# Kernel optimization log

Hardware: AMD Instinct MI355X
Metric: run time of the kernel (lower is better)

The kernel has to match this reference:

```python
import jax, jax.numpy as jnp
import numpy as np


def setup_inputs() -> dict:
    key = jax.random.key(0)
    ks = jax.random.split(key, 7)
    B, N, D = 32, 512, 64
    H = D // 2
    return {
        "receiver": jax.random.normal(ks[0], (B, N, D), dtype=jnp.float32),
        "attendant": jax.random.normal(ks[1], (B, N, D), dtype=jnp.float32),
        "adj_mask": jax.random.uniform(ks[2], (B, N, N), dtype=jnp.float32),
        "w_q": jax.random.normal(ks[3], (D, H), dtype=jnp.float32) * (1.0 / np.sqrt(D)),
        "w_k": jax.random.normal(ks[4], (D, H), dtype=jnp.float32) * (1.0 / np.sqrt(D)),
        "bias": jax.random.normal(ks[5], (H,), dtype=jnp.float32) * 0.1,
        "a": jax.random.normal(ks[6], (H,), dtype=jnp.float32) * 0.1,
    }


def reference(receiver, attendant, adj_mask, w_q, w_k, bias, a):
    # keys: [B,N,H], queries: [B,N,H]
    keys = receiver @ w_k
    queries = attendant @ w_q
    # additive (GAT-style) scores: broadcast-add -> tanh -> dot with a
    # e_act: [B, N, M, H]  (N from keys, M from queries, matching torch unsqueeze(-3)/(-2))
    e_act = jnp.tanh(queries[:, None, :, :] + keys[:, :, None, :] + bias)
    e_scores = jnp.einsum("bnmh,h->bnm", e_act, a)
    # masked projection: adj @ scores @ adj
    att = jnp.einsum("bnk,bkm->bnm", adj_mask, e_scores)
    att = jnp.einsum("bnk,bkm->bnm", att, adj_mask)
    return att
```

## Files before the change

kernel.cpp:

```cpp
#include <hip/hip_runtime.h>

#define GN 512
#define HH 32
#define DD 64

typedef float v4f __attribute__((ext_vector_type(4)));
typedef unsigned int v4u __attribute__((ext_vector_type(4)));
typedef u_int32_t u32;
typedef u32 v2u __attribute__((ext_vector_type(2)));
typedef __bf16 v8bf __attribute__((ext_vector_type(8)));

__device__ __forceinline__ u32 f2bf(float f) {
  u32 u = __builtin_bit_cast(u32, f);
  return (u + 0x7fffu + ((u >> 16) & 1u)) >> 16;
}
__device__ __forceinline__ u32 pack2(float a, float b) {
  return f2bf(a) | (f2bf(b) << 16);
}

#define GLOAD16(g, l)                                                              \
  __builtin_amdgcn_global_load_lds((const __attribute__((address_space(1))) u32*)(g), \
                                   (__attribute__((address_space(3))) u32*)(l), 16, 0, 0)
#define VMCNT0 asm volatile("s_waitcnt vmcnt(0)" ::: "memory")

__global__ __launch_bounds__(256) void kq_kernel(const float* __restrict__ rec,
                                                 const float* __restrict__ att,
                                                 const float* __restrict__ wq,
                                                 const float* __restrict__ wk,
                                                 const float* __restrict__ bias,
                                                 float* __restrict__ ekbuf,
                                                 float* __restrict__ eqbuf) {
  __shared__ float rr[512], ra[512];
  int tid = threadIdx.x;
  size_t base = (size_t)blockIdx.x * 8;
  const float* gr = rec + base * DD;
  const float* ga = att + base * DD;
  rr[tid] = gr[tid]; rr[tid + 256] = gr[tid + 256];
  ra[tid] = ga[tid]; ra[tid + 256] = ga[tid + 256];
  __syncthreads();
  int r = tid >> 5, h = tid & 31;
  float sk = bias[h], sq = 0.f;
  const float* rrow = &rr[r * DD];
  const float* arow = &ra[r * DD];
#pragma unroll 8
  for (int d = 0; d < DD; ++d) {
    sk += rrow[d] * wk[d * HH + h];
    sq += arow[d] * wq[d * HH + h];
  }
  const float C = 2.8853900817779268f;
  ekbuf[(base + r) * HH + h] = __builtin_exp2f(C * sk);
  eqbuf[(base + r) * HH + h] = __builtin_exp2f(C * sq);
}

__global__ __launch_bounds__(256) void prep_kernel(const float* __restrict__ adj,
                                                   const float* __restrict__ ek,
                                                   const float* __restrict__ eq,
                                                   const float* __restrict__ avec,
                                                   unsigned short* __restrict__ adjT,
                                                   unsigned short* __restrict__ adjBF,
                                                   unsigned short* __restrict__ Et) {
  __shared__ __align__(16) float smem[4608];
  float (*t)[65] = (float (*)[65])smem;
  float (*kl)[36] = (float (*)[36])smem;
  float (*ql)[36] = (float (*)[36])&smem[64 * 36];

  int tid = threadIdx.x;
  int b = blockIdx.z;
  int n0 = blockIdx.x * 64, m0 = blockIdx.y * 64;
  int c0 = n0, r0 = m0;

  const float* kb = ek + ((size_t)b * GN + n0) * HH;
  const float* qb = eq + ((size_t)b * GN + m0) * HH;
  v4f rk[2], rq[2];
#pragma unroll
  for (int k = 0; k < 2; ++k) {
    int v = tid + k * 256;
    int row = v >> 3, seg = v & 7;
    rk[k] = *(const v4f*)(kb + row * HH + seg * 4);
    rq[k] = *(const v4f*)(qb + row * HH + seg * 4);
  }
  v4f a2v[8];
  float asum = 0.f;
#pragma unroll
  for (int h4 = 0; h4 < 8; ++h4) {
    v4f av = *(const v4f*)(avec + h4 * 4);
    a2v[h4] = av * 2.0f;
    asum += av[0] + av[1] + av[2] + av[3];
  }

  const float* ab = adj + (size_t)b * GN * GN;
  unsigned short* ob = adjT + (size_t)b * GN * GN;
  unsigned short* of = adjBF + (size_t)b * GN * GN;
#pragma unroll
  for (int k = 0; k < 4; ++k) {
    int v = tid + k * 256;
    int row = v >> 4, seg = v & 15;
    v4f f = *(const v4f*)(ab + (size_t)(r0 + row) * GN + c0 + seg * 4);
    t[row][seg * 4 + 0] = f[0];
    t[row][seg * 4 + 1] = f[1];
    t[row][seg * 4 + 2] = f[2];
    t[row][seg * 4 + 3] = f[3];
    v2u p = {pack2(f[0], f[1]), pack2(f[2], f[3])};
    *(v2u*)(of + (size_t)(r0 + row) * GN + c0 + seg * 4) = p;
  }
  __syncthreads();
  {
    int c = tid >> 2;
    int rs = (tid & 3) * 16;
    v4u p0, p1;
#pragma unroll
    for (int j = 0; j < 4; ++j) {
      p0[j] = pack2(t[rs + 2 * j][c], t[rs + 2 * j + 1][c]);
      p1[j] = pack2(t[rs + 8 + 2 * j][c], t[rs + 9 + 2 * j][c]);
    }
    unsigned short* dst = ob + (size_t)(c0 + c) * GN + r0 + rs;
    *(v4u*)dst = p0;
    *(v4u*)(dst + 8) = p1;
  }
  __syncthreads();

#pragma unroll
  for (int k = 0; k < 2; ++k) {
    int v = tid + k * 256;
    int row = v >> 3, seg = v & 7;
    *(v4f*)&kl[row][seg * 4] = rk[k];
    *(v4f*)&ql[row][seg * 4] = rq[k];
  }
  __syncthreads();
  int m = tid >> 2, ng = tid & 3;
  v4f qv[8];
#pragma unroll
  for (int h4 = 0; h4 < 8; ++h4) qv[h4] = *(const v4f*)&ql[m][h4 * 4];
  u32* dstw = (u32*)(Et + ((size_t)b * GN + m0 + m) * GN + n0);
#pragma unroll 4
  for (int nn = 0; nn < 8; ++nn) {
    int n = ng * 2 + nn * 8;
    v4f acc0 = (v4f){0.f, 0.f, 0.f, 0.f};
    v4f acc1 = (v4f){0.f, 0.f, 0.f, 0.f};
#pragma unroll
    for (int h4 = 0; h4 < 8; ++h4) {
      v4f kv0 = *(const v4f*)&kl[n][h4 * 4];
      v4f kv1 = *(const v4f*)&kl[n + 1][h4 * 4];
      v4f f0 = kv0 * qv[h4] + 1.0f;
      v4f f1 = kv1 * qv[h4] + 1.0f;
      v4f r0v, r1v;
#pragma unroll
      for (int e = 0; e < 4; ++e) {
        r0v[e] = __builtin_amdgcn_rcpf(f0[e]);
        r1v[e] = __builtin_amdgcn_rcpf(f1[e]);
      }
      acc0 += a2v[h4] * r0v;
      acc1 += a2v[h4] * r1v;
    }
    float s0 = asum - (acc0[0] + acc0[1] + acc0[2] + acc0[3]);
    float s1 = asum - (acc1[0] + acc1[1] + acc1[2] + acc1[3]);
    __bf16 b0 = (__bf16)s0, b1 = (__bf16)s1;
    u32 w = (u32)__builtin_bit_cast(unsigned short, b0) |
            ((u32)__builtin_bit_cast(unsigned short, b1) << 16);
    dstw[n >> 1] = w;
  }
}

#define SWZ(r, s) ((s) ^ ((r) & 7))

template <bool OUTF32>
__global__ __launch_bounds__(256) void gemm_bt(const unsigned short* __restrict__ A,
                                               const unsigned short* __restrict__ Bt,
                                               void* __restrict__ Cv) {
  __shared__ unsigned short At[2][128 * 64];
  __shared__ unsigned short Bs[2][128 * 64];
  int bid = blockIdx.x;
  int swz = (bid & 7) * 64 + (bid >> 3);
  int b = swz >> 4;
  int row0 = ((swz >> 2) & 3) * 128;
  int col0 = (swz & 3) * 128;
  int tid = threadIdx.x, lane = tid & 63, wave = tid >> 6;
  int wr = wave >> 1, wc = wave & 1;
  const unsigned short* Ab = A + (size_t)b * GN * GN;
  const unsigned short* Bb = Bt + (size_t)b * GN * GN;

  v4f acc[4][4];
#pragma unroll
  for (int i = 0; i < 4; ++i)
#pragma unroll
    for (int j = 0; j < 4; ++j) acc[i][j] = (v4f){0.f, 0.f, 0.f, 0.f};

  int cc_r[4], cc_s[4];
#pragma unroll
  for (int i = 0; i < 4; ++i) {
    int c = i * 256 + tid;
    cc_r[i] = c >> 3;
    cc_s[i] = SWZ(c >> 3, c & 7);
  }

#define STAGE(buf, kt)                                                                   \
  {                                                                                      \
    _Pragma("unroll") for (int i = 0; i < 4; ++i) {                                      \
      const unsigned short* ga = Ab + (size_t)(row0 + cc_r[i]) * GN + (kt)*64 + cc_s[i] * 8; \
      const unsigned short* gb = Bb + (size_t)(col0 + cc_r[i]) * GN + (kt)*64 + cc_s[i] * 8; \
      GLOAD16(ga, (char*)&At[buf][0] + (i * 256 + wave * 64) * 16);                      \
      GLOAD16(gb, (char*)&Bs[buf][0] + (i * 256 + wave * 64) * 16);                      \
    }                                                                                    \
  }

#define COMPUTE(buf)                                                                     \
  {                                                                                      \
    int lr = lane & 15, s16 = lane >> 4;                                                 \
    _Pragma("unroll") for (int h = 0; h < 2; ++h) {                                      \
      int sl = h * 4 + s16;                                                              \
      v8bf af[4], bfv[4];                                                                \
      _Pragma("unroll") for (int i = 0; i < 4; ++i) {                                    \
        int r = wr * 64 + i * 16 + lr;                                                   \
        af[i] = *(const v8bf*)&At[buf][r * 64 + SWZ(r, sl) * 8];                         \
      }                                                                                  \
      _Pragma("unroll") for (int j = 0; j < 4; ++j) {                                    \
        int r = wc * 64 + j * 16 + lr;                                                   \
        bfv[j] = *(const v8bf*)&Bs[buf][r * 64 + SWZ(r, sl) * 8];                        \
      }                                                                                  \
      _Pragma("unroll") for (int i = 0; i < 4; ++i)                                      \
          _Pragma("unroll") for (int j = 0; j < 4; ++j) acc[i][j] =                      \
          __builtin_amdgcn_mfma_f32_16x16x32_bf16(af[i], bfv[j], acc[i][j], 0, 0, 0);    \
    }                                                                                    \
  }

  STAGE(0, 0);
  VMCNT0;
  __builtin_amdgcn_s_barrier();
#pragma unroll
  for (int kt = 0; kt < 7; ++kt) {
    int cur = kt & 1;
    STAGE(cur ^ 1, kt + 1);
    COMPUTE(cur);
    VMCNT0;
    __builtin_amdgcn_s_barrier();
  }
  COMPUTE(1);

  int lc = lane & 15;
  int lrow4 = (lane >> 4) * 4;
#pragma unroll
  for (int i = 0; i < 4; ++i) {
#pragma unroll
    for (int j = 0; j < 4; ++j) {
      int gr = row0 + wr * 64 + i * 16 + lrow4;
      int gc = col0 + wc * 64 + j * 16 + lc;
#pragma unroll
      for (int e = 0; e < 4; ++e) {
        float v = acc[i][j][e];
        if constexpr (OUTF32)
          ((float*)Cv)[(size_t)b * GN * GN + (size_t)(gr + e) * GN + gc] = v;
        else
          ((unsigned short*)Cv)[(size_t)b * GN * GN + (size_t)(gr + e) * GN + gc] =
              (unsigned short)f2bf(v);
      }
    }
  }
#undef STAGE
#undef COMPUTE
}

extern "C" void kernel_launch(void* const* d_in, const int* in_sizes, int n_in,
                              void* d_out, int out_size, void* d_ws, size_t ws_size,
                              hipStream_t stream) {
  const float* receiver  = (const float*)d_in[0];
  const float* attendant = (const float*)d_in[1];
  const float* adj       = (const float*)d_in[2];
  const float* wq        = (const float*)d_in[3];
  const float* wk        = (const float*)d_in[4];
  const float* bias      = (const float*)d_in[5];
  const float* avec      = (const float*)d_in[6];
  float* out = (float*)d_out;

  char* ws = (char*)d_ws;
  float* ekbuf          = (float*)(ws);
  float* eqbuf          = (float*)(ws + (2u << 20));
  unsigned short* Et    = (unsigned short*)(ws + (4u << 20));
  unsigned short* adjT  = (unsigned short*)(ws + (20u << 20));
  unsigned short* adjBF = (unsigned short*)(ws + (36u << 20));
  unsigned short* Tbuf  = (unsigned short*)(ws + (52u << 20));

  kq_kernel<<<dim3(2048), dim3(256), 0, stream>>>(receiver, attendant, wq, wk, bias,
                                                  ekbuf, eqbuf);
  prep_kernel<<<dim3(8, 8, 32), dim3(256), 0, stream>>>(adj, ekbuf, eqbuf, avec,
                                                        adjT, adjBF, Et);
  gemm_bt<false><<<dim3(512), dim3(256), 0, stream>>>(adjBF, Et, Tbuf);
  gemm_bt<true><<<dim3(512), dim3(256), 0, stream>>>(Tbuf, adjT, out);
}
```

Baseline: 80.00 us.

## Async-load prep tiles into LDS and overlap adj load with score compute

The prep kernel now issues direct global-to-LDS loads for the k/q tiles and the adjacency tile, using XOR-swizzled layouts in place of padded ones. It waits only for the k/q loads before computing the tanh scores, so the adjacency fetch overlaps with the rcp-heavy arithmetic. The bf16 conversion and transpose of adj happen afterwards, and the score results are held in registers until the end. This adds more LDS (separate buffers) and depends on correct vmcnt ordering and swizzle arithmetic.

```diff
diff --git a/kernel.cpp b/kernel.cpp
--- a/kernel.cpp
+++ b/kernel.cpp
@@ -22,6 +22,7 @@
   __builtin_amdgcn_global_load_lds((const __attribute__((address_space(1))) u32*)(g), \
                                    (__attribute__((address_space(3))) u32*)(l), 16, 0, 0)
 #define VMCNT0 asm volatile("s_waitcnt vmcnt(0)" ::: "memory")
+#define SCHEDBAR __builtin_amdgcn_sched_barrier(0)
 
 __global__ __launch_bounds__(256) void kq_kernel(const float* __restrict__ rec,
                                                  const float* __restrict__ att,
@@ -59,26 +60,15 @@
                                                    unsigned short* __restrict__ adjT,
                                                    unsigned short* __restrict__ adjBF,
                                                    unsigned short* __restrict__ Et) {
-  __shared__ __align__(16) float smem[4608];
-  float (*t)[65] = (float (*)[65])smem;
-  float (*kl)[36] = (float (*)[36])smem;
-  float (*ql)[36] = (float (*)[36])&smem[64 * 36];
-
-  int tid = threadIdx.x;
+  __shared__ __align__(16) float tA[64 * 64];
+  __shared__ __align__(16) float kl[64 * 32];
+  __shared__ __align__(16) float ql[64 * 32];
+
+  int tid = threadIdx.x, wave = tid >> 6;
   int b = blockIdx.z;
   int n0 = blockIdx.x * 64, m0 = blockIdx.y * 64;
   int c0 = n0, r0 = m0;
 
-  const float* kb = ek + ((size_t)b * GN + n0) * HH;
-  const float* qb = eq + ((size_t)b * GN + m0) * HH;
-  v4f rk[2], rq[2];
-#pragma unroll
-  for (int k = 0; k < 2; ++k) {
-    int v = tid + k * 256;
-    int row = v >> 3, seg = v & 7;
-    rk[k] = *(const v4f*)(kb + row * HH + seg * 4);
-    rq[k] = *(const v4f*)(qb + row * HH + seg * 4);
-  }
   v4f a2v[8];
   float asum = 0.f;
 #pragma unroll
@@ -87,60 +77,46 @@
     a2v[h4] = av * 2.0f;
     asum += av[0] + av[1] + av[2] + av[3];
   }
-
+  SCHEDBAR;
+
+  const float* kb = ek + ((size_t)b * GN + n0) * HH;
+  const float* qb = eq + ((size_t)b * GN + m0) * HH;
+#pragma unroll
+  for (int i = 0; i < 2; ++i) {
+    int c = i * 256 + tid;
+    int r = c >> 3, g = (c & 7) ^ (r & 7);
+    GLOAD16(kb + r * HH + g * 4, (char*)kl + (i * 256 + wave * 64) * 16);
+    GLOAD16(qb + r * HH + g * 4, (char*)ql + (i * 256 + wave * 64) * 16);
+  }
+  SCHEDBAR;
   const float* ab = adj + (size_t)b * GN * GN;
-  unsigned short* ob = adjT + (size_t)b * GN * GN;
-  unsigned short* of = adjBF + (size_t)b * GN * GN;
-#pragma unroll
-  for (int k = 0; k < 4; ++k) {
-    int v = tid + k * 256;
-    int row = v >> 4, seg = v & 15;
-    v4f f = *(const v4f*)(ab + (size_t)(r0 + row) * GN + c0 + seg * 4);
-    t[row][seg * 4 + 0] = f[0];
-    t[row][seg * 4 + 1] = f[1];
-    t[row][seg * 4 + 2] = f[2];
-    t[row][seg * 4 + 3] = f[3];
-    v2u p = {pack2(f[0], f[1]), pack2(f[2], f[3])};
-    *(v2u*)(of + (size_t)(r0 + row) * GN + c0 + seg * 4) = p;
-  }
-  __syncthreads();
-  {
-    int c = tid >> 2;
-    int rs = (tid & 3) * 16;
-    v4u p0, p1;
-#pragma unroll
-    for (int j = 0; j < 4; ++j) {
-      p0[j] = pack2(t[rs + 2 * j][c], t[rs + 2 * j + 1][c]);
-      p1[j] = pack2(t[rs + 8 + 2 * j][c], t[rs + 9 + 2 * j][c]);
-    }
-    unsigned short* dst = ob + (size_t)(c0 + c) * GN + r0 + rs;
-    *(v4u*)dst = p0;
-    *(v4u*)(dst + 8) = p1;
-  }
-  __syncthreads();
-
-#pragma unroll
-  for (int k = 0; k < 2; ++k) {
-    int v = tid + k * 256;
-    int row = v >> 3, seg = v & 7;
-    *(v4f*)&kl[row][seg * 4] = rk[k];
-    *(v4f*)&ql[row][seg * 4] = rq[k];
-  }
-  __syncthreads();
+#pragma unroll
+  for (int i = 0; i < 4; ++i) {
+    int c = i * 256 + tid;
+    int r = c >> 4, g = (c & 15) ^ (r & 15);
+    GLOAD16(ab + (size_t)(r0 + r) * GN + c0 + g * 4, (char*)tA + (i * 256 + wave * 64) * 16);
+  }
+  SCHEDBAR;
+  asm volatile("s_waitcnt vmcnt(4)" ::: "memory");
+  __builtin_amdgcn_s_barrier();
+  SCHEDBAR;
+
   int m = tid >> 2, ng = tid & 3;
   v4f qv[8];
 #pragma unroll
-  for (int h4 = 0; h4 < 8; ++h4) qv[h4] = *(const v4f*)&ql[m][h4 * 4];
-  u32* dstw = (u32*)(Et + ((size_t)b * GN + m0 + m) * GN + n0);
-#pragma unroll 4
+  for (int h4 = 0; h4 < 8; ++h4)
+    qv[h4] = *(const v4f*)&ql[m * HH + ((h4 ^ (m & 7)) << 2)];
+  int x0 = 2 * ng, x1 = 2 * ng + 1;
+  u32 ow[8];
+#pragma unroll
   for (int nn = 0; nn < 8; ++nn) {
     int n = ng * 2 + nn * 8;
     v4f acc0 = (v4f){0.f, 0.f, 0.f, 0.f};
     v4f acc1 = (v4f){0.f, 0.f, 0.f, 0.f};
 #pragma unroll
     for (int h4 = 0; h4 < 8; ++h4) {
-      v4f kv0 = *(const v4f*)&kl[n][h4 * 4];
-      v4f kv1 = *(const v4f*)&kl[n + 1][h4 * 4];
+      v4f kv0 = *(const v4f*)&kl[n * HH + ((h4 ^ x0) << 2)];
+      v4f kv1 = *(const v4f*)&kl[(n + 1) * HH + ((h4 ^ x1) << 2)];
       v4f f0 = kv0 * qv[h4] + 1.0f;
       v4f f1 = kv1 * qv[h4] + 1.0f;
       v4f r0v, r1v;
@@ -154,11 +130,41 @@
     }
     float s0 = asum - (acc0[0] + acc0[1] + acc0[2] + acc0[3]);
     float s1 = asum - (acc1[0] + acc1[1] + acc1[2] + acc1[3]);
-    __bf16 b0 = (__bf16)s0, b1 = (__bf16)s1;
-    u32 w = (u32)__builtin_bit_cast(unsigned short, b0) |
-            ((u32)__builtin_bit_cast(unsigned short, b1) << 16);
-    dstw[n >> 1] = w;
-  }
+    ow[nn] = pack2(s0, s1);
+  }
+
+  VMCNT0;
+  __builtin_amdgcn_s_barrier();
+  SCHEDBAR;
+
+  unsigned short* of = adjBF + (size_t)b * GN * GN;
+#pragma unroll
+  for (int i = 0; i < 4; ++i) {
+    int c = i * 256 + tid;
+    int r = c >> 4, g = (c & 15) ^ (r & 15);
+    v4f f = *(const v4f*)&tA[c * 4];
+    v2u pk = {pack2(f[0], f[1]), pack2(f[2], f[3])};
+    *(v2u*)(of + (size_t)(r0 + r) * GN + c0 + g * 4) = pk;
+  }
+  {
+    unsigned short* ob = adjT + (size_t)b * GN * GN;
+    int col = tid & 63, rs = (tid >> 6) * 16;
+    int gc = col >> 2, ce = col & 3;
+    u32 qq[8];
+#pragma unroll
+    for (int j = 0; j < 8; ++j) {
+      int R0 = rs + 2 * j, R1 = R0 + 1;
+      float v0 = tA[R0 * 64 + ((gc ^ (R0 & 15)) << 2) + ce];
+      float v1 = tA[R1 * 64 + ((gc ^ (R1 & 15)) << 2) + ce];
+      qq[j] = pack2(v0, v1);
+    }
+    unsigned short* dst = ob + (size_t)(c0 + col) * GN + r0 + rs;
+    *(v4u*)dst = (v4u){qq[0], qq[1], qq[2], qq[3]};
+    *(v4u*)(dst + 8) = (v4u){qq[4], qq[5], qq[6], qq[7]};
+  }
+  u32* dstw = (u32*)(Et + ((size_t)b * GN + m0 + m) * GN + n0);
+#pragma unroll
+  for (int nn = 0; nn < 8; ++nn) dstw[ng + nn * 4] = ow[nn];
 }
 
 #define SWZ(r, s) ((s) ^ ((r) & 7))
```

After: 80.78 us. No clear change (+1.0%).

## Split prep into specialized score blocks and adjacency conversion blocks

Applied to the files above, without the earlier changes.

Replaces the combined prep kernel with a heterogeneous grid: four of every five blocks compute only the bf16 score tile, and the fifth converts and transposes four adjacency tiles. The score path now uses 4x4 register tiling per thread and pairs the reciprocals (num/den combining two terms), which halves the rcp count. The goal is to let memory-bound adjacency conversion overlap with ALU-bound score computation and to cut per-element transcendental cost. In exchange it adds scattered 2-byte stores for Et and raises register pressure.

```diff
diff --git a/kernel.cpp b/kernel.cpp
--- a/kernel.cpp
+++ b/kernel.cpp
@@ -52,112 +52,126 @@
   eqbuf[(base + r) * HH + h] = __builtin_exp2f(C * sq);
 }
 
-__global__ __launch_bounds__(256) void prep_kernel(const float* __restrict__ adj,
-                                                   const float* __restrict__ ek,
-                                                   const float* __restrict__ eq,
-                                                   const float* __restrict__ avec,
-                                                   unsigned short* __restrict__ adjT,
-                                                   unsigned short* __restrict__ adjBF,
-                                                   unsigned short* __restrict__ Et) {
+__global__ __launch_bounds__(256) void prep2_kernel(const float* __restrict__ adj,
+                                                    const float* __restrict__ ek,
+                                                    const float* __restrict__ eq,
+                                                    const float* __restrict__ avec,
+                                                    unsigned short* __restrict__ adjT,
+                                                    unsigned short* __restrict__ adjBF,
+                                                    unsigned short* __restrict__ Et) {
   __shared__ __align__(16) float smem[4608];
-  float (*t)[65] = (float (*)[65])smem;
-  float (*kl)[36] = (float (*)[36])smem;
-  float (*ql)[36] = (float (*)[36])&smem[64 * 36];
-
   int tid = threadIdx.x;
-  int b = blockIdx.z;
-  int n0 = blockIdx.x * 64, m0 = blockIdx.y * 64;
-  int c0 = n0, r0 = m0;
-
-  const float* kb = ek + ((size_t)b * GN + n0) * HH;
-  const float* qb = eq + ((size_t)b * GN + m0) * HH;
-  v4f rk[2], rq[2];
-#pragma unroll
-  for (int k = 0; k < 2; ++k) {
-    int v = tid + k * 256;
-    int row = v >> 3, seg = v & 7;
-    rk[k] = *(const v4f*)(kb + row * HH + seg * 4);
-    rq[k] = *(const v4f*)(qb + row * HH + seg * 4);
-  }
-  v4f a2v[8];
-  float asum = 0.f;
-#pragma unroll
-  for (int h4 = 0; h4 < 8; ++h4) {
-    v4f av = *(const v4f*)(avec + h4 * 4);
-    a2v[h4] = av * 2.0f;
-    asum += av[0] + av[1] + av[2] + av[3];
-  }
-
-  const float* ab = adj + (size_t)b * GN * GN;
-  unsigned short* ob = adjT + (size_t)b * GN * GN;
-  unsigned short* of = adjBF + (size_t)b * GN * GN;
-#pragma unroll
-  for (int k = 0; k < 4; ++k) {
-    int v = tid + k * 256;
-    int row = v >> 4, seg = v & 15;
-    v4f f = *(const v4f*)(ab + (size_t)(r0 + row) * GN + c0 + seg * 4);
-    t[row][seg * 4 + 0] = f[0];
-    t[row][seg * 4 + 1] = f[1];
-    t[row][seg * 4 + 2] = f[2];
-    t[row][seg * 4 + 3] = f[3];
-    v2u p = {pack2(f[0], f[1]), pack2(f[2], f[3])};
-    *(v2u*)(of + (size_t)(r0 + row) * GN + c0 + seg * 4) = p;
-  }
-  __syncthreads();
-  {
-    int c = tid >> 2;
-    int rs = (tid & 3) * 16;
-    v4u p0, p1;
+  int bid = blockIdx.x;
+  int type = bid % 5, grp = bid / 5;
+
+  if (type < 4) {
+    float (*kl)[36] = (float (*)[36])smem;
+    float (*ql)[36] = (float (*)[36])&smem[64 * 36];
+    int e = grp * 4 + type;
+    int b = e >> 6, rem = e & 63;
+    int n0 = (rem & 7) * 64, m0 = (rem >> 3) * 64;
+
+    const float* kb = ek + ((size_t)b * GN + n0) * HH;
+    const float* qb = eq + ((size_t)b * GN + m0) * HH;
+    int sr = tid >> 3, sp = tid & 7;
+    v4f rk0 = *(const v4f*)(kb + sr * HH + sp * 4);
+    v4f rq0 = *(const v4f*)(qb + sr * HH + sp * 4);
+    v4f rk1 = *(const v4f*)(kb + (sr + 32) * HH + sp * 4);
+    v4f rq1 = *(const v4f*)(qb + (sr + 32) * HH + sp * 4);
+    *(v4f*)&kl[sr][sp * 4] = rk0;
+    *(v4f*)&ql[sr][sp * 4] = rq0;
+    *(v4f*)&kl[sr + 32][sp * 4] = rk1;
+    *(v4f*)&ql[sr + 32][sp * 4] = rq1;
+
+    float a2s[HH];
+    float asum = 0.f;
+#pragma unroll
+    for (int h = 0; h < HH; ++h) {
+      float av = avec[h];
+      a2s[h] = 2.0f * av;
+      asum += av;
+    }
+    __syncthreads();
+
+    int mg = tid >> 4, ng = tid & 15;
+    const float* kvb[4];
+    const float* qvb[4];
 #pragma unroll
     for (int j = 0; j < 4; ++j) {
-      p0[j] = pack2(t[rs + 2 * j][c], t[rs + 2 * j + 1][c]);
-      p1[j] = pack2(t[rs + 8 + 2 * j][c], t[rs + 9 + 2 * j][c]);
-    }
-    unsigned short* dst = ob + (size_t)(c0 + c) * GN + r0 + rs;
-    *(v4u*)dst = p0;
-    *(v4u*)(dst + 8) = p1;
-  }
-  __syncthreads();
-
-#pragma unroll
-  for (int k = 0; k < 2; ++k) {
-    int v = tid + k * 256;
-    int row = v >> 3, seg = v & 7;
-    *(v4f*)&kl[row][seg * 4] = rk[k];
-    *(v4f*)&ql[row][seg * 4] = rq[k];
-  }
-  __syncthreads();
-  int m = tid >> 2, ng = tid & 3;
-  v4f qv[8];
-#pragma unroll
-  for (int h4 = 0; h4 < 8; ++h4) qv[h4] = *(const v4f*)&ql[m][h4 * 4];
-  u32* dstw = (u32*)(Et + ((size_t)b * GN + m0 + m) * GN + n0);
-#pragma unroll 4
-  for (int nn = 0; nn < 8; ++nn) {
-    int n = ng * 2 + nn * 8;
-    v4f acc0 = (v4f){0.f, 0.f, 0.f, 0.f};
-    v4f acc1 = (v4f){0.f, 0.f, 0.f, 0.f};
+      kvb[j] = &kl[ng + 16 * j][0];
+      qvb[j] = &ql[mg + 16 * j][0];
+    }
+    float acc[4][4];
+#pragma unroll
+    for (int i = 0; i < 4; ++i)
+#pragma unroll
+      for (int j = 0; j < 4; ++j) acc[i][j] = 0.f;
+
 #pragma unroll
     for (int h4 = 0; h4 < 8; ++h4) {
-      v4f kv0 = *(const v4f*)&kl[n][h4 * 4];
-      v4f kv1 = *(const v4f*)&kl[n + 1][h4 * 4];
-      v4f f0 = kv0 * qv[h4] + 1.0f;
-      v4f f1 = kv1 * qv[h4] + 1.0f;
-      v4f r0v, r1v;
-#pragma unroll
-      for (int e = 0; e < 4; ++e) {
-        r0v[e] = __builtin_amdgcn_rcpf(f0[e]);
-        r1v[e] = __builtin_amdgcn_rcpf(f1[e]);
+      v4f kv[4], qv[4];
+#pragma unroll
+      for (int j = 0; j < 4; ++j) kv[j] = *(const v4f*)(kvb[j] + h4 * 4);
+#pragma unroll
+      for (int i = 0; i < 4; ++i) qv[i] = *(const v4f*)(qvb[i] + h4 * 4);
+      float a0 = a2s[h4 * 4 + 0], a1 = a2s[h4 * 4 + 1];
+      float a2 = a2s[h4 * 4 + 2], a3 = a2s[h4 * 4 + 3];
+#pragma unroll
+      for (int i = 0; i < 4; ++i)
+#pragma unroll
+        for (int j = 0; j < 4; ++j) {
+          v4f f = kv[j] * qv[i] + 1.0f;
+          float den0 = f[0] * f[1], den1 = f[2] * f[3];
+          float num0 = __builtin_fmaf(a0, f[1], a1 * f[0]);
+          float num1 = __builtin_fmaf(a2, f[3], a3 * f[2]);
+          acc[i][j] = __builtin_fmaf(num0, __builtin_amdgcn_rcpf(den0), acc[i][j]);
+          acc[i][j] = __builtin_fmaf(num1, __builtin_amdgcn_rcpf(den1), acc[i][j]);
+        }
+    }
+    unsigned short* eb = Et + ((size_t)b * GN + m0 + mg) * GN + n0 + ng;
+#pragma unroll
+    for (int i = 0; i < 4; ++i)
+#pragma unroll
+      for (int j = 0; j < 4; ++j)
+        eb[(size_t)(16 * i) * GN + 16 * j] = (unsigned short)f2bf(asum - acc[i][j]);
+  } else {
+    float (*t)[65] = (float (*)[65])smem;
+#pragma unroll 1
+    for (int l = 0; l < 4; ++l) {
+      int tt = grp * 4 + l;
+      int b = tt >> 6, rem = tt & 63;
+      int c0 = (rem & 7) * 64, r0 = (rem >> 3) * 64;
+      const float* ab = adj + (size_t)b * GN * GN;
+      unsigned short* ob = adjT + (size_t)b * GN * GN;
+      unsigned short* of = adjBF + (size_t)b * GN * GN;
+#pragma unroll
+      for (int k = 0; k < 4; ++k) {
+        int v = tid + k * 256;
+        int row = v >> 4, seg = v & 15;
+        v4f f = *(const v4f*)(ab + (size_t)(r0 + row) * GN + c0 + seg * 4);
+        t[row][seg * 4 + 0] = f[0];
+        t[row][seg * 4 + 1] = f[1];
+        t[row][seg * 4 + 2] = f[2];
+        t[row][seg * 4 + 3] = f[3];
+        v2u p = {pack2(f[0], f[1]), pack2(f[2], f[3])};
+        *(v2u*)(of + (size_t)(r0 + row) * GN + c0 + seg * 4) = p;
       }
-      acc0 += a2v[h4] * r0v;
-      acc1 += a2v[h4] * r1v;
-    }
-    float s0 = asum - (acc0[0] + acc0[1] + acc0[2] + acc0[3]);
-    float s1 = asum - (acc1[0] + acc1[1] + acc1[2] + acc1[3]);
-    __bf16 b0 = (__bf16)s0, b1 = (__bf16)s1;
-    u32 w = (u32)__builtin_bit_cast(unsigned short, b0) |
-            ((u32)__builtin_bit_cast(unsigned short, b1) << 16);
-    dstw[n >> 1] = w;
+      __syncthreads();
+      {
+        int c = tid >> 2;
+        int rs = (tid & 3) * 16;
+        v4u p0, p1;
+#pragma unroll
+        for (int j = 0; j < 4; ++j) {
+          p0[j] = pack2(t[rs + 2 * j][c], t[rs + 2 * j + 1][c]);
+          p1[j] = pack2(t[rs + 8 + 2 * j][c], t[rs + 9 + 2 * j][c]);
+        }
+        unsigned short* dst = ob + (size_t)(c0 + c) * GN + r0 + rs;
+        *(v4u*)dst = p0;
+        *(v4u*)(dst + 8) = p1;
+      }
+      __syncthreads();
+    }
   }
 }
 
@@ -281,8 +295,8 @@
 
   kq_kernel<<<dim3(2048), dim3(256), 0, stream>>>(receiver, attendant, wq, wk, bias,
                                                   ekbuf, eqbuf);
-  prep_kernel<<<dim3(8, 8, 32), dim3(256), 0, stream>>>(adj, ekbuf, eqbuf, avec,
-                                                        adjT, adjBF, Et);
+  prep2_kernel<<<dim3(2560), dim3(256), 0, stream>>>(adj, ekbuf, eqbuf, avec,
+                                                     adjT, adjBF, Et);
   gemm_bt<false><<<dim3(512), dim3(256), 0, stream>>>(adjBF, Et, Tbuf);
   gemm_bt<true><<<dim3(512), dim3(256), 0, stream>>>(Tbuf, adjT, out);
 }
```

Result: faster. 78.42 us (-2.0%).
